# Optimization experiments

Hardware: AMD Instinct MI355X
Metric: run time of the kernel (lower is better)

The kernel has to match this reference:

```python
import jax, jax.numpy as jnp
from jax import lax
import numpy as np

NDIM = 256
BATCH = 65536
NROT = NDIM * (NDIM - 1) // 2  # comb(ndim, 2) = 32640


def _givens_mat(rots, ii, jj, ndim):
    """Product G_last @ ... @ G_1 of Givens rotations in combinations order.

    Left-multiplying by G(i, j, theta) only modifies rows i and j, so we apply
    each rotation as a rank-2 row update instead of a full matmul (same math
    as the original `plane_rot_mat @ mat` loop).
    """
    def step(mat, carry):
        i, j, th = carry
        c = jnp.cos(th)
        s = jnp.sin(th)
        ri = mat[i]
        rj = mat[j]
        mat = mat.at[i].set(c * ri - s * rj)
        mat = mat.at[j].set(s * ri + c * rj)
        return mat, None

    mat0 = jnp.eye(ndim, dtype=jnp.complex64)
    mat, _ = lax.scan(step, mat0, (ii, jj, rots))
    return mat


def setup_inputs() -> dict:
    key = jax.random.key(0)
    k1, k2, k3, k4 = jax.random.split(key, 4)
    x = jax.random.normal(k1, (BATCH, NDIM), dtype=jnp.float32)
    rots1 = 0.1 * jax.random.normal(k2, (NROT,), dtype=jnp.float32)
    phases = 0.1 * jax.random.normal(k3, (NDIM,), dtype=jnp.float32)
    rots2 = 0.1 * jax.random.normal(k4, (NROT,), dtype=jnp.float32)
    return {"x": x, "rots1": rots1, "phases": phases, "rots2": rots2}


def reference(x, rots1, phases, rots2):
    ndim = x.shape[1]
    # np.triu_indices(ndim, 1) enumerates (i, j) pairs in the same row-major
    # order as itertools.combinations(range(ndim), 2).
    ii_np, jj_np = np.triu_indices(ndim, k=1)
    ii = jnp.asarray(ii_np, dtype=jnp.int32)
    jj = jnp.asarray(jj_np, dtype=jnp.int32)

    # vector_norm: row-wise L2 normalization
    xn = x / jnp.linalg.norm(x, axis=1, keepdims=True)
    xc = xn.astype(jnp.complex64)

    # rot1: y = x @ M1.T with M1 = G_last @ ... @ G_1
    M1 = _givens_mat(rots1, ii, jj, ndim)
    y = xc @ M1.T

    # phase_transforms: x @ diag(exp(i*phases)) == elementwise phase multiply
    y = y * jnp.exp(1j * phases)

    # rot2
    M2 = _givens_mat(rots2, ii, jj, ndim)
    y = y @ M2.T

    # measure: |.|^2
    return jnp.abs(y) ** 2
```

## Files before the change

### kernel.cpp

```cpp
#include <hip/hip_runtime.h>
#include <stdint.h>
#include <math.h>

#define NDIM 256
#define BATCH 65536
#define NROT 32640

typedef float  f32x4 __attribute__((ext_vector_type(4)));
typedef short  s16x8 __attribute__((ext_vector_type(8)));
typedef unsigned int u32x4 __attribute__((ext_vector_type(4)));
typedef unsigned int u32x2 __attribute__((ext_vector_type(2)));

static __device__ __forceinline__ unsigned short f2bf(float f) {
    unsigned int u = __float_as_uint(f);
    u += 0x7fffu + ((u >> 16) & 1u);
    return (unsigned short)(u >> 16);
}

static __device__ __forceinline__ int sweep_bound(int k, int pblk) {
    int target = k * (NROT / pblk);
    int best = 0, bd = 0x7fffffff;
    for (int i = 0; i <= 256; i += 4) {
        int pre = i * 255 - (i * (i - 1)) / 2;
        int d = pre - target; d = (d < 0) ? -d : d;
        if (d < bd) { bd = d; best = i; }
    }
    return best;
}

__global__ __launch_bounds__(64) void k_blocks(const float* __restrict__ r1,
                                               const float* __restrict__ r2,
                                               float* __restrict__ bmats, int pblk) {
    __shared__ float colb[264 * 64];
    __shared__ float2 csb[256 * 4];
    __shared__ float2 tri[24 * 6];
    const int t = threadIdx.x;
    const int chunk = blockIdx.x;
    const int b = blockIdx.y;
    const int set = blockIdx.z;
    const int col0 = chunk * 64;
    const float* rots = set ? r2 : r1;

    const int s0 = sweep_bound(b, pblk);
    const int s1 = sweep_bound(b + 1, pblk);
    const int ngroups = (s1 - s0) >> 2;

    {
        const f32x4 z = {0.f, 0.f, 0.f, 0.f};
        #pragma unroll 11
        for (int q = 0; q < 66; q++)
            *(f32x4*)&colb[(q * 64 + t) * 4] = z;
        colb[(col0 + t) * 64 + t] = 1.0f;
    }

    for (int k = t; k < ngroups * 6; k += 64) {
        int g = k / 6, q = k - g * 6;
        int a  = (q < 3) ? 0 : ((q < 5) ? 1 : 2);
        int bb = (q < 3) ? (q + 1) : ((q < 5) ? (q - 1) : 3);
        int m0 = s0 + g * 4;
        int m = m0 + a;
        int base = m * 255 - (m * (m - 1)) / 2;
        float th = rots[base - m - 1 + (m0 + bb)];
        float sv, cv; sincosf(th, &sv, &cv);
        tri[k] = make_float2(cv, sv);
    }

    for (int g = 0; g < ngroups; g++) {
        const int m0 = s0 + g * 4;
        int off[4];
        #pragma unroll
        for (int a = 0; a < 4; a++) {
            int m = m0 + a;
            int base = m * 255 - (m * (m - 1)) / 2;
            off[a] = base - m - 1;
        }
        const int n_j = 252 - m0;
        const int n_p = (n_j > 0) ? ((n_j + 7) & ~7) : 0;

        for (int k = t; k < n_p * 4; k += 64) {
            int jj = k >> 2, a = k & 3;
            int j = m0 + 4 + jj;
            if (j < 256) {
                float th = rots[off[a] + j];
                float sv, cv; sincosf(th, &sv, &cv);
                csb[k] = make_float2(cv, sv);
            } else {
                csb[k] = make_float2(1.f, 0.f);
            }
        }

        float u0 = colb[(m0 + 0) * 64 + t];
        float u1 = colb[(m0 + 1) * 64 + t];
        float u2 = colb[(m0 + 2) * 64 + t];
        float u3 = colb[(m0 + 3) * 64 + t];

        {
            float2 cv; float nr;
            cv = tri[g * 6 + 0]; nr = cv.y * u0 + cv.x * u1; u0 = cv.x * u0 - cv.y * u1; u1 = nr;
            cv = tri[g * 6 + 1]; nr = cv.y * u0 + cv.x * u2; u0 = cv.x * u0 - cv.y * u2; u2 = nr;
            cv = tri[g * 6 + 2]; nr = cv.y * u0 + cv.x * u3; u0 = cv.x * u0 - cv.y * u3; u3 = nr;
            cv = tri[g * 6 + 3]; nr = cv.y * u1 + cv.x * u2; u1 = cv.x * u1 - cv.y * u2; u2 = nr;
            cv = tri[g * 6 + 4]; nr = cv.y * u1 + cv.x * u3; u1 = cv.x * u1 - cv.y * u3; u3 = nr;
            cv = tri[g * 6 + 5]; nr = cv.y * u2 + cv.x * u3; u2 = cv.x * u2 - cv.y * u3; u3 = nr;
        }

        if (n_p > 0) {
            float rbuf[8];
            #pragma unroll
            for (int p = 0; p < 8; p++)
                rbuf[p] = colb[(m0 + 4 + p) * 64 + t];
            for (int c = 0; c < n_p; c += 8) {
                #pragma unroll
                for (int p = 0; p < 8; p++) {
                    const int j = m0 + 4 + c + p;
                    float r = rbuf[p];
                    int jn = j + 8; jn = (jn < 263) ? jn : 263;
                    rbuf[p] = colb[jn * 64 + t];
                    float2 a0 = csb[(c + p) * 4 + 0];
                    float2 a1 = csb[(c + p) * 4 + 1];
                    float2 a2 = csb[(c + p) * 4 + 2];
                    float2 a3 = csb[(c + p) * 4 + 3];
                    float nr;
                    nr = a0.y * u0 + a0.x * r; u0 = a0.x * u0 - a0.y * r; r = nr;
                    nr = a1.y * u1 + a1.x * r; u1 = a1.x * u1 - a1.y * r; r = nr;
                    nr = a2.y * u2 + a2.x * r; u2 = a2.x * u2 - a2.y * r; r = nr;
                    nr = a3.y * u3 + a3.x * r; u3 = a3.x * u3 - a3.y * r; r = nr;
                    colb[j * 64 + t] = r;
                }
            }
        }
        colb[(m0 + 0) * 64 + t] = u0;
        colb[(m0 + 1) * 64 + t] = u1;
        colb[(m0 + 2) * 64 + t] = u2;
        colb[(m0 + 3) * 64 + t] = u3;
    }

    float* outm = bmats + (size_t)(set * pblk + b) * 65536;
    for (int r = 0; r < 256; r++)
        outm[(size_t)r * 256 + col0 + t] = colb[r * 64 + t];
}

__global__ __launch_bounds__(256) void k_combine(const float* __restrict__ src,
                                                 float* __restrict__ dst,
                                                 int half, int pblk) {
    const int by = blockIdx.y;
    const int set = by / half, pidx = by % half;
    const int stride = pblk / (2 * half);
    const int s0A = sweep_bound((2 * pidx + 1) * stride, pblk);
    const float* Am = src + (size_t)(set * 2 * half + 2 * pidx + 1) * 65536;
    const float* Bm = src + (size_t)(set * 2 * half + 2 * pidx) * 65536;
    float* Dm = dst + (size_t)(set * half + pidx) * 65536;
    const int tr = blockIdx.x >> 2, tc = blockIdx.x & 3;
    const int tid = threadIdx.x;

    if (tr * 64 + 64 <= s0A) {
        #pragma unroll
        for (int it = 0; it < 4; it++) {
            int flat = tid + it * 256;
            int r = flat >> 4, c4 = flat & 15;
            size_t idx = (size_t)(tr * 64 + r) * 256 + tc * 64 + c4 * 4;
            *(f32x4*)&Dm[idx] = *(const f32x4*)&Bm[idx];
        }
        return;
    }
    const int kb0 = (tr * 64 >= s0A) ? (s0A >> 5) : 0;

    __shared__ float As[64 * 36];
    __shared__ float Bs[32 * 64];
    const int tx = tid & 15, ty = tid >> 4;

    float acc[4][4] = {};
    for (int kb = kb0; kb < 8; kb++) {
        __syncthreads();
        #pragma unroll
        for (int it = 0; it < 2; it++) {
            int flat = tid + it * 256;
            int r = flat >> 3, c4 = flat & 7;
            f32x4 v = *(const f32x4*)&Am[(size_t)(tr * 64 + r) * 256 + kb * 32 + c4 * 4];
            *(f32x4*)&As[r * 36 + c4 * 4] = v;
        }
        #pragma unroll
        for (int it = 0; it < 2; it++) {
            int flat = tid + it * 256;
            int r = flat >> 4, c4 = flat & 15;
            f32x4 v = *(const f32x4*)&Bm[(size_t)(kb * 32 + r) * 256 + tc * 64 + c4 * 4];
            *(f32x4*)&Bs[r * 64 + c4 * 4] = v;
        }
        __syncthreads();
        #pragma unroll 8
        for (int kk = 0; kk < 32; kk++) {
            f32x4 bv = *(const f32x4*)&Bs[kk * 64 + tx * 4];
            float a0 = As[(ty * 4 + 0) * 36 + kk];
            float a1 = As[(ty * 4 + 1) * 36 + kk];
            float a2 = As[(ty * 4 + 2) * 36 + kk];
            float a3 = As[(ty * 4 + 3) * 36 + kk];
            #pragma unroll
            for (int j = 0; j < 4; j++) {
                acc[0][j] += a0 * bv[j];
                acc[1][j] += a1 * bv[j];
                acc[2][j] += a2 * bv[j];
                acc[3][j] += a3 * bv[j];
            }
        }
    }
    #pragma unroll
    for (int i = 0; i < 4; i++) {
        f32x4 v = { acc[i][0], acc[i][1], acc[i][2], acc[i][3] };
        *(f32x4*)&Dm[(size_t)(tr * 64 + ty * 4 + i) * 256 + tc * 64 + tx * 4] = v;
    }
}

__global__ __launch_bounds__(256) void k_abt(const float* __restrict__ mats,
                                             const float* __restrict__ phases,
                                             unsigned short* __restrict__ abt) {
    const float* Am = mats + 65536;
    const float* Bm = mats;
    const int v = blockIdx.y;
    const int tr = blockIdx.x >> 2, tc = blockIdx.x & 3;

    __shared__ float As[64 * 36];
    __shared__ float Bs[32 * 64];
    const int tid = threadIdx.x;
    const int tx = tid & 15, ty = tid >> 4;

    float acc[4][4] = {};
    for (int kb = 0; kb < 8; kb++) {
        __syncthreads();
        #pragma unroll
        for (int it = 0; it < 2; it++) {
            int flat = tid + it * 256;
            int r = flat >> 3, c4 = flat & 7;
            f32x4 vv = *(const f32x4*)&Am[(size_t)(tr * 64 + r) * 256 + kb * 32 + c4 * 4];
            *(f32x4*)&As[r * 36 + c4 * 4] = vv;
        }
        #pragma unroll
        for (int it = 0; it < 2; it++) {
            int flat = tid + it * 256;
            int r = flat >> 4, c4 = flat & 15;
            int kg = kb * 32 + r;
            float ph = phases[kg];
            float sc = v ? sinf(ph) : cosf(ph);
            f32x4 vv = *(const f32x4*)&Bm[(size_t)kg * 256 + tc * 64 + c4 * 4];
            vv[0] *= sc; vv[1] *= sc; vv[2] *= sc; vv[3] *= sc;
            *(f32x4*)&Bs[r * 64 + c4 * 4] = vv;
        }
        __syncthreads();
        #pragma unroll 8
        for (int kk = 0; kk < 32; kk++) {
            f32x4 bv = *(const f32x4*)&Bs[kk * 64 + tx * 4];
            float a0 = As[(ty * 4 + 0) * 36 + kk];
            float a1 = As[(ty * 4 + 1) * 36 + kk];
            float a2 = As[(ty * 4 + 2) * 36 + kk];
            float a3 = As[(ty * 4 + 3) * 36 + kk];
            #pragma unroll
            for (int j = 0; j < 4; j++) {
                acc[0][j] += a0 * bv[j];
                acc[1][j] += a1 * bv[j];
                acc[2][j] += a2 * bv[j];
                acc[3][j] += a3 * bv[j];
            }
        }
    }
    #pragma unroll
    for (int i = 0; i < 4; i++) {
        unsigned short h0 = f2bf(acc[i][0]), h1 = f2bf(acc[i][1]);
        unsigned short h2 = f2bf(acc[i][2]), h3 = f2bf(acc[i][3]);
        u32x2 pk = { (unsigned)h0 | ((unsigned)h1 << 16),
                     (unsigned)h2 | ((unsigned)h3 << 16) };
        *(u32x2*)&abt[(size_t)(v * 256 + tr * 64 + ty * 4 + i) * 256 + tc * 64 + tx * 4] = pk;
    }
}

__global__ __launch_bounds__(256) void k_xnorm(const float* __restrict__ x,
                                               unsigned short* __restrict__ xbf) {
    const int row = blockIdx.x * 4 + (threadIdx.x >> 6);
    const int lane = threadIdx.x & 63;
    f32x4 v = *(const f32x4*)&x[(size_t)row * 256 + lane * 4];
    float s = v[0] * v[0] + v[1] * v[1] + v[2] * v[2] + v[3] * v[3];
    for (int off = 32; off; off >>= 1) s += __shfl_xor(s, off, 64);
    float sc = 1.0f / sqrtf(s);
    unsigned short h0 = f2bf(v[0] * sc), h1 = f2bf(v[1] * sc);
    unsigned short h2 = f2bf(v[2] * sc), h3 = f2bf(v[3] * sc);
    u32x2 pk = { (unsigned)h0 | ((unsigned)h1 << 16),
                 (unsigned)h2 | ((unsigned)h3 << 16) };
    *(u32x2*)&xbf[(size_t)row * 256 + lane * 4] = pk;
}

__global__ __launch_bounds__(256) void k_norm(const float* __restrict__ x,
                                              float* __restrict__ invn) {
    const int row = blockIdx.x * 4 + (threadIdx.x >> 6);
    const int lane = threadIdx.x & 63;
    f32x4 v = *(const f32x4*)&x[(size_t)row * 256 + lane * 4];
    float s = v[0] * v[0] + v[1] * v[1] + v[2] * v[2] + v[3] * v[3];
    for (int off = 32; off; off >>= 1) s += __shfl_xor(s, off, 64);
    if (lane == 0) invn[row] = 1.0f / sqrtf(s);
}

#define BKP 136
__global__ __launch_bounds__(256) void k_gemm_bf(const unsigned short* __restrict__ xbf,
                                                 const unsigned short* __restrict__ abt,
                                                 float* __restrict__ out) {
    __shared__ unsigned short As[128 * BKP];
    __shared__ unsigned short Bs[128 * BKP];
    const int tid = threadIdx.x;
    const int cb = blockIdx.x;
    const int rb = blockIdx.y;
    const int lane = tid & 63, w = tid >> 6;

    f32x4 acc[16];
    #pragma unroll
    for (int i = 0; i < 16; i++) acc[i] = (f32x4){0.f, 0.f, 0.f, 0.f};

    int rA[8], cA[8], grB[8];
    #pragma unroll
    for (int it = 0; it < 8; it++) {
        int flat = tid + it * 256;
        rA[it] = flat >> 4; cA[it] = flat & 15;
        int r = rA[it];
        grB[it] = (r < 64) ? (cb * 64 + r) : (256 + cb * 64 + (r - 64));
    }

    u32x4 pa[8], pb[8];
    #pragma unroll
    for (int it = 0; it < 8; it++) {
        pa[it] = *(const u32x4*)&xbf[(size_t)(rb * 128 + rA[it]) * 256 + cA[it] * 8];
        pb[it] = *(const u32x4*)&abt[(size_t)grB[it] * 256 + cA[it] * 8];
    }
    #pragma unroll
    for (int it = 0; it < 8; it++) {
        *(u32x4*)&As[rA[it] * BKP + cA[it] * 8] = pa[it];
        *(u32x4*)&Bs[rA[it] * BKP + cA[it] * 8] = pb[it];
    }
    __syncthreads();
    #pragma unroll
    for (int it = 0; it < 8; it++) {
        pa[it] = *(const u32x4*)&xbf[(size_t)(rb * 128 + rA[it]) * 256 + 128 + cA[it] * 8];
        pb[it] = *(const u32x4*)&abt[(size_t)grB[it] * 256 + 128 + cA[it] * 8];
    }

    auto compute = [&]() {
        #pragma unroll
        for (int ks = 0; ks < 4; ks++) {
            const int k0 = ks * 32 + (lane >> 4) * 8;
            s16x8 a[2], b[8];
            #pragma unroll
            for (int tm = 0; tm < 2; tm++)
                a[tm] = *(const s16x8*)&As[(w * 32 + tm * 16 + (lane & 15)) * BKP + k0];
            #pragma unroll
            for (int tn = 0; tn < 8; tn++)
                b[tn] = *(const s16x8*)&Bs[(tn * 16 + (lane & 15)) * BKP + k0];
            #pragma unroll
            for (int tm = 0; tm < 2; tm++)
                #pragma unroll
                for (int tn = 0; tn < 8; tn++)
                    acc[tm * 8 + tn] = __builtin_amdgcn_mfma_f32_16x16x32_bf16(
                        a[tm], b[tn], acc[tm * 8 + tn], 0, 0, 0);
        }
    };
    compute();
    __syncthreads();
    #pragma unroll
    for (int it = 0; it < 8; it++) {
        *(u32x4*)&As[rA[it] * BKP + cA[it] * 8] = pa[it];
        *(u32x4*)&Bs[rA[it] * BKP + cA[it] * 8] = pb[it];
    }
    __syncthreads();
    compute();

    const int qr = lane >> 4, c = lane & 15;
    #pragma unroll
    for (int tm = 0; tm < 2; tm++) {
        #pragma unroll
        for (int tn = 0; tn < 4; tn++) {
            f32x4 p = acc[tm * 8 + tn];
            f32x4 q = acc[tm * 8 + tn + 4];
            #pragma unroll
            for (int r = 0; r < 4; r++) {
                int m = w * 32 + tm * 16 + qr * 4 + r;
                out[(size_t)(rb * 128 + m) * 256 + cb * 64 + tn * 16 + c] =
                    p[r] * p[r] + q[r] * q[r];
            }
        }
    }
}

__global__ __launch_bounds__(256) void k_gemm_f32(const float* __restrict__ x,
                                                  const unsigned short* __restrict__ abt,
                                                  const float* __restrict__ invn,
                                                  float* __restrict__ out) {
    __shared__ unsigned short As[128 * BKP];
    __shared__ unsigned short Bs[128 * BKP];
    const int tid = threadIdx.x;
    const int cb = blockIdx.x;
    const int rb = blockIdx.y;
    const int lane = tid & 63, w = tid >> 6;

    f32x4 acc[16];
    #pragma unroll
    for (int i = 0; i < 16; i++) acc[i] = (f32x4){0.f, 0.f, 0.f, 0.f};

    for (int kb = 0; kb < 2; kb++) {
        __syncthreads();
        #pragma unroll
        for (int it = 0; it < 16; it++) {
            int flat = tid + it * 256;
            int r = flat >> 5, c4 = flat & 31;
            f32x4 v = *(const f32x4*)&x[(size_t)(rb * 128 + r) * 256 + kb * 128 + c4 * 4];
            float sc = invn[rb * 128 + r];
            v[0] *= sc; v[1] *= sc; v[2] *= sc; v[3] *= sc;
            unsigned short h0 = f2bf(v[0]), h1 = f2bf(v[1]);
            unsigned short h2 = f2bf(v[2]), h3 = f2bf(v[3]);
            u32x2 pk = { (unsigned)h0 | ((unsigned)h1 << 16),
                         (unsigned)h2 | ((unsigned)h3 << 16) };
            *(u32x2*)&As[r * BKP + c4 * 4] = pk;
        }
        #pragma unroll
        for (int it = 0; it < 8; it++) {
            int flat = tid + it * 256;
            int r = flat >> 4, c8 = flat & 15;
            int gr = (r < 64) ? (cb * 64 + r) : (256 + cb * 64 + (r - 64));
            u32x4 vv = *(const u32x4*)&abt[(size_t)gr * 256 + kb * 128 + c8 * 8];
            *(u32x4*)&Bs[r * BKP + c8 * 8] = vv;
        }
        __syncthreads();
        #pragma unroll
        for (int ks = 0; ks < 4; ks++) {
            const int k0 = ks * 32 + (lane >> 4) * 8;
            s16x8 a[2], b[8];
            #pragma unroll
            for (int tm = 0; tm < 2; tm++)
                a[tm] = *(const s16x8*)&As[(w * 32 + tm * 16 + (lane & 15)) * BKP + k0];
            #pragma unroll
            for (int tn = 0; tn < 8; tn++)
                b[tn] = *(const s16x8*)&Bs[(tn * 16 + (lane & 15)) * BKP + k0];
            #pragma unroll
            for (int tm = 0; tm < 2; tm++)
                #pragma unroll
                for (int tn = 0; tn < 8; tn++)
                    acc[tm * 8 + tn] = __builtin_amdgcn_mfma_f32_16x16x32_bf16(
                        a[tm], b[tn], acc[tm * 8 + tn], 0, 0, 0);
        }
    }

    const int qr = lane >> 4, c = lane & 15;
    #pragma unroll
    for (int tm = 0; tm < 2; tm++) {
        #pragma unroll
        for (int tn = 0; tn < 4; tn++) {
            f32x4 p = acc[tm * 8 + tn];
            f32x4 q = acc[tm * 8 + tn + 4];
            #pragma unroll
            for (int r = 0; r < 4; r++) {
                int m = w * 32 + tm * 16 + qr * 4 + r;
                out[(size_t)(rb * 128 + m) * 256 + cb * 64 + tn * 16 + c] =
                    p[r] * p[r] + q[r] * q[r];
            }
        }
    }
}

extern "C" void kernel_launch(void* const* d_in, const int* in_sizes, int n_in,
                              void* d_out, int out_size, void* d_ws, size_t ws_size,
                              hipStream_t stream) {
    (void)in_sizes; (void)n_in; (void)out_size;
    const float* x      = (const float*)d_in[0];
    const float* rots1  = (const float*)d_in[1];
    const float* phases = (const float*)d_in[2];
    const float* rots2  = (const float*)d_in[3];
    float* out = (float*)d_out;
    char* ws = (char*)d_ws;

    const size_t MAT = 262144;
    int pblk = 32;
    while (pblk > 16 &&
           (size_t)3 * pblk * MAT + 2 * MAT + (size_t)BATCH * 512 > ws_size)
        pblk >>= 1;
    const size_t offA   = 0;
    const size_t offB   = offA + (size_t)2 * pblk * MAT;
    const size_t offABT = offB + (size_t)pblk * MAT;
    const size_t offINV = offABT + MAT;
    const size_t offXBF = offINV + MAT;
    const bool use_xbf = (offXBF + (size_t)BATCH * 512) <= ws_size;

    float*          A    = (float*)(ws + offA);
    float*          B    = (float*)(ws + offB);
    unsigned short* abt  = (unsigned short*)(ws + offABT);
    float*          invn = (float*)(ws + offINV);
    unsigned short* xbf  = (unsigned short*)(ws + offXBF);

    k_blocks<<<dim3(4, pblk, 2), 64, 0, stream>>>(rots1, rots2, A, pblk);

    float* srcp = A; float* dstp = B;
    for (int half = pblk / 2; half >= 1; half >>= 1) {
        k_combine<<<dim3(16, 2 * half), 256, 0, stream>>>(srcp, dstp, half, pblk);
        float* tmp = srcp; srcp = dstp; dstp = tmp;
    }
    k_abt<<<dim3(16, 2), 256, 0, stream>>>(srcp, phases, abt);

    if (use_xbf) {
        k_xnorm<<<BATCH / 4, 256, 0, stream>>>(x, xbf);
        k_gemm_bf<<<dim3(4, BATCH / 128), 256, 0, stream>>>(xbf, abt, out);
    } else {
        k_norm<<<BATCH / 4, 256, 0, stream>>>(x, invn);
        k_gemm_f32<<<dim3(4, BATCH / 128), 256, 0, stream>>>(x, abt, invn, out);
    }
}
```

Before: 323.1 us.

## Use split-bf16 MFMA in combine/abt GEMMs and fold x normalization into k_blocks

The small 256x256 matrix products in k_combine and k_abt move from scalar FP32 FMA loops to bf16 MFMA instructions. Each operand is split into high and low bf16 parts and three MFMAs are issued per tile, so the products stay close to FP32 accuracy. The row normalization of x is merged into the k_blocks launch as extra blocks, which removes a kernel launch and lets that memory-bound work overlap the serial Givens block computation. This adds split and conversion overhead plus a strided B load, and the three-term split loses some precision compared with FP32.

```diff
diff --git a/kernel.cpp b/kernel.cpp
--- a/kernel.cpp
+++ b/kernel.cpp
@@ -15,6 +15,38 @@
     unsigned int u = __float_as_uint(f);
     u += 0x7fffu + ((u >> 16) & 1u);
     return (unsigned short)(u >> 16);
+}
+static __device__ __forceinline__ float bf2f(unsigned short h) {
+    return __uint_as_float(((unsigned)h) << 16);
+}
+
+static __device__ __forceinline__ void split4(f32x4 v, u32x2* hi, u32x2* lo) {
+    unsigned short h[4], l[4];
+    #pragma unroll
+    for (int i = 0; i < 4; i++) {
+        h[i] = f2bf(v[i]);
+        l[i] = f2bf(v[i] - bf2f(h[i]));
+    }
+    *hi = (u32x2){ (unsigned)h[0] | ((unsigned)h[1] << 16),
+                   (unsigned)h[2] | ((unsigned)h[3] << 16) };
+    *lo = (u32x2){ (unsigned)l[0] | ((unsigned)l[1] << 16),
+                   (unsigned)l[2] | ((unsigned)l[3] << 16) };
+}
+static __device__ __forceinline__ void split8(const float* v, u32x4* hi, u32x4* lo) {
+    unsigned short h[8], l[8];
+    #pragma unroll
+    for (int i = 0; i < 8; i++) {
+        h[i] = f2bf(v[i]);
+        l[i] = f2bf(v[i] - bf2f(h[i]));
+    }
+    *hi = (u32x4){ (unsigned)h[0] | ((unsigned)h[1] << 16),
+                   (unsigned)h[2] | ((unsigned)h[3] << 16),
+                   (unsigned)h[4] | ((unsigned)h[5] << 16),
+                   (unsigned)h[6] | ((unsigned)h[7] << 16) };
+    *lo = (u32x4){ (unsigned)l[0] | ((unsigned)l[1] << 16),
+                   (unsigned)l[2] | ((unsigned)l[3] << 16),
+                   (unsigned)l[4] | ((unsigned)l[5] << 16),
+                   (unsigned)l[6] | ((unsigned)l[7] << 16) };
 }
 
 static __device__ __forceinline__ int sweep_bound(int k, int pblk) {
@@ -30,14 +62,45 @@
 
 __global__ __launch_bounds__(64) void k_blocks(const float* __restrict__ r1,
                                                const float* __restrict__ r2,
-                                               float* __restrict__ bmats, int pblk) {
+                                               float* __restrict__ bmats, int pblk,
+                                               const float* __restrict__ xg,
+                                               unsigned short* __restrict__ xbf) {
     __shared__ float colb[264 * 64];
     __shared__ float2 csb[256 * 4];
     __shared__ float2 tri[24 * 6];
+    const int nblk = 8 * pblk;
+
+    if ((int)blockIdx.x >= nblk) {
+        const int lane = threadIdx.x;
+        const int r0 = ((int)blockIdx.x - nblk) * 16;
+        #pragma unroll
+        for (int hb = 0; hb < 2; hb++) {
+            f32x4 v[8];
+            #pragma unroll
+            for (int i = 0; i < 8; i++)
+                v[i] = *(const f32x4*)&xg[(size_t)(r0 + hb * 8 + i) * 256 + lane * 4];
+            #pragma unroll
+            for (int i = 0; i < 8; i++) {
+                float s = v[i][0] * v[i][0] + v[i][1] * v[i][1]
+                        + v[i][2] * v[i][2] + v[i][3] * v[i][3];
+                #pragma unroll
+                for (int off = 32; off; off >>= 1) s += __shfl_xor(s, off, 64);
+                float sc = 1.0f / sqrtf(s);
+                unsigned short h0 = f2bf(v[i][0] * sc), h1 = f2bf(v[i][1] * sc);
+                unsigned short h2 = f2bf(v[i][2] * sc), h3 = f2bf(v[i][3] * sc);
+                u32x2 pk = { (unsigned)h0 | ((unsigned)h1 << 16),
+                             (unsigned)h2 | ((unsigned)h3 << 16) };
+                *(u32x2*)&xbf[(size_t)(r0 + hb * 8 + i) * 256 + lane * 4] = pk;
+            }
+        }
+        return;
+    }
+
     const int t = threadIdx.x;
-    const int chunk = blockIdx.x;
-    const int b = blockIdx.y;
-    const int set = blockIdx.z;
+    const int bid = blockIdx.x;
+    const int chunk = bid & 3;
+    const int b = (bid >> 2) % pblk;
+    const int set = (bid >> 2) / pblk;
     const int col0 = chunk * 64;
     const float* rots = set ? r2 : r1;
 
@@ -165,11 +228,20 @@
     }
     const int kb0 = (tr * 64 >= s0A) ? (s0A >> 5) : 0;
 
-    __shared__ float As[64 * 36];
-    __shared__ float Bs[32 * 64];
-    const int tx = tid & 15, ty = tid >> 4;
-
-    float acc[4][4] = {};
+    __shared__ unsigned short Ahi[64 * 40], Alo[64 * 40];
+    __shared__ unsigned short Bhi[64 * 40], Blo[64 * 40];
+
+    const int lane = tid & 63, w = tid >> 6;
+    const int mh = (w >> 1) * 32, nh = (w & 1) * 32;
+    const int l15 = lane & 15, lq = lane >> 4;
+    const int bn = tid & 63, bkq = tid >> 6;
+
+    f32x4 acc[2][2];
+    #pragma unroll
+    for (int i = 0; i < 2; i++)
+        #pragma unroll
+        for (int j = 0; j < 2; j++) acc[i][j] = (f32x4){0.f, 0.f, 0.f, 0.f};
+
     for (int kb = kb0; kb < 8; kb++) {
         __syncthreads();
         #pragma unroll
@@ -177,37 +249,48 @@
             int flat = tid + it * 256;
             int r = flat >> 3, c4 = flat & 7;
             f32x4 v = *(const f32x4*)&Am[(size_t)(tr * 64 + r) * 256 + kb * 32 + c4 * 4];
-            *(f32x4*)&As[r * 36 + c4 * 4] = v;
-        }
-        #pragma unroll
-        for (int it = 0; it < 2; it++) {
-            int flat = tid + it * 256;
-            int r = flat >> 4, c4 = flat & 15;
-            f32x4 v = *(const f32x4*)&Bm[(size_t)(kb * 32 + r) * 256 + tc * 64 + c4 * 4];
-            *(f32x4*)&Bs[r * 64 + c4 * 4] = v;
+            u32x2 hi, lo; split4(v, &hi, &lo);
+            *(u32x2*)&Ahi[r * 40 + c4 * 4] = hi;
+            *(u32x2*)&Alo[r * 40 + c4 * 4] = lo;
+        }
+        {
+            float bv[8];
+            #pragma unroll
+            for (int i = 0; i < 8; i++)
+                bv[i] = Bm[(size_t)(kb * 32 + bkq * 8 + i) * 256 + tc * 64 + bn];
+            u32x4 hi, lo; split8(bv, &hi, &lo);
+            *(u32x4*)&Bhi[bn * 40 + bkq * 8] = hi;
+            *(u32x4*)&Blo[bn * 40 + bkq * 8] = lo;
         }
         __syncthreads();
-        #pragma unroll 8
-        for (int kk = 0; kk < 32; kk++) {
-            f32x4 bv = *(const f32x4*)&Bs[kk * 64 + tx * 4];
-            float a0 = As[(ty * 4 + 0) * 36 + kk];
-            float a1 = As[(ty * 4 + 1) * 36 + kk];
-            float a2 = As[(ty * 4 + 2) * 36 + kk];
-            float a3 = As[(ty * 4 + 3) * 36 + kk];
-            #pragma unroll
-            for (int j = 0; j < 4; j++) {
-                acc[0][j] += a0 * bv[j];
-                acc[1][j] += a1 * bv[j];
-                acc[2][j] += a2 * bv[j];
-                acc[3][j] += a3 * bv[j];
-            }
-        }
-    }
-    #pragma unroll
-    for (int i = 0; i < 4; i++) {
-        f32x4 v = { acc[i][0], acc[i][1], acc[i][2], acc[i][3] };
-        *(f32x4*)&Dm[(size_t)(tr * 64 + ty * 4 + i) * 256 + tc * 64 + tx * 4] = v;
-    }
+        s16x8 ah[2], al[2], bh[2], bl[2];
+        #pragma unroll
+        for (int tm = 0; tm < 2; tm++) {
+            ah[tm] = *(const s16x8*)&Ahi[(mh + tm * 16 + l15) * 40 + lq * 8];
+            al[tm] = *(const s16x8*)&Alo[(mh + tm * 16 + l15) * 40 + lq * 8];
+        }
+        #pragma unroll
+        for (int tn = 0; tn < 2; tn++) {
+            bh[tn] = *(const s16x8*)&Bhi[(nh + tn * 16 + l15) * 40 + lq * 8];
+            bl[tn] = *(const s16x8*)&Blo[(nh + tn * 16 + l15) * 40 + lq * 8];
+        }
+        #pragma unroll
+        for (int tm = 0; tm < 2; tm++)
+            #pragma unroll
+            for (int tn = 0; tn < 2; tn++) {
+                acc[tm][tn] = __builtin_amdgcn_mfma_f32_16x16x32_bf16(ah[tm], bh[tn], acc[tm][tn], 0, 0, 0);
+                acc[tm][tn] = __builtin_amdgcn_mfma_f32_16x16x32_bf16(ah[tm], bl[tn], acc[tm][tn], 0, 0, 0);
+                acc[tm][tn] = __builtin_amdgcn_mfma_f32_16x16x32_bf16(al[tm], bh[tn], acc[tm][tn], 0, 0, 0);
+            }
+    }
+    #pragma unroll
+    for (int tm = 0; tm < 2; tm++)
+        #pragma unroll
+        for (int tn = 0; tn < 2; tn++)
+            #pragma unroll
+            for (int r = 0; r < 4; r++)
+                Dm[(size_t)(tr * 64 + mh + tm * 16 + lq * 4 + r) * 256
+                   + tc * 64 + nh + tn * 16 + l15] = acc[tm][tn][r];
 }
 
 __global__ __launch_bounds__(256) void k_abt(const float* __restrict__ mats,
@@ -217,13 +300,22 @@
     const float* Bm = mats;
     const int v = blockIdx.y;
     const int tr = blockIdx.x >> 2, tc = blockIdx.x & 3;
-
-    __shared__ float As[64 * 36];
-    __shared__ float Bs[32 * 64];
     const int tid = threadIdx.x;
-    const int tx = tid & 15, ty = tid >> 4;
-
-    float acc[4][4] = {};
+
+    __shared__ unsigned short Ahi[64 * 40], Alo[64 * 40];
+    __shared__ unsigned short Bhi[64 * 40], Blo[64 * 40];
+
+    const int lane = tid & 63, w = tid >> 6;
+    const int mh = (w >> 1) * 32, nh = (w & 1) * 32;
+    const int l15 = lane & 15, lq = lane >> 4;
+    const int bn = tid & 63, bkq = tid >> 6;
+
+    f32x4 acc[2][2];
+    #pragma unroll
+    for (int i = 0; i < 2; i++)
+        #pragma unroll
+        for (int j = 0; j < 2; j++) acc[i][j] = (f32x4){0.f, 0.f, 0.f, 0.f};
+
     for (int kb = 0; kb < 8; kb++) {
         __syncthreads();
         #pragma unroll
@@ -231,59 +323,52 @@
             int flat = tid + it * 256;
             int r = flat >> 3, c4 = flat & 7;
             f32x4 vv = *(const f32x4*)&Am[(size_t)(tr * 64 + r) * 256 + kb * 32 + c4 * 4];
-            *(f32x4*)&As[r * 36 + c4 * 4] = vv;
-        }
-        #pragma unroll
-        for (int it = 0; it < 2; it++) {
-            int flat = tid + it * 256;
-            int r = flat >> 4, c4 = flat & 15;
-            int kg = kb * 32 + r;
-            float ph = phases[kg];
-            float sc = v ? sinf(ph) : cosf(ph);
-            f32x4 vv = *(const f32x4*)&Bm[(size_t)kg * 256 + tc * 64 + c4 * 4];
-            vv[0] *= sc; vv[1] *= sc; vv[2] *= sc; vv[3] *= sc;
-            *(f32x4*)&Bs[r * 64 + c4 * 4] = vv;
+            u32x2 hi, lo; split4(vv, &hi, &lo);
+            *(u32x2*)&Ahi[r * 40 + c4 * 4] = hi;
+            *(u32x2*)&Alo[r * 40 + c4 * 4] = lo;
+        }
+        {
+            float bv[8];
+            #pragma unroll
+            for (int i = 0; i < 8; i++) {
+                int kg = kb * 32 + bkq * 8 + i;
+                float ph = phases[kg];
+                float sc = v ? sinf(ph) : cosf(ph);
+                bv[i] = Bm[(size_t)kg * 256 + tc * 64 + bn] * sc;
+            }
+            u32x4 hi, lo; split8(bv, &hi, &lo);
+            *(u32x4*)&Bhi[bn * 40 + bkq * 8] = hi;
+            *(u32x4*)&Blo[bn * 40 + bkq * 8] = lo;
         }
         __syncthreads();
-        #pragma unroll 8
-        for (int kk = 0; kk < 32; kk++) {
-            f32x4 bv = *(const f32x4*)&Bs[kk * 64 + tx * 4];
-            float a0 = As[(ty * 4 + 0) * 36 + kk];
-            float a1 = As[(ty * 4 + 1) * 36 + kk];
-            float a2 = As[(ty * 4 + 2) * 36 + kk];
-            float a3 = As[(ty * 4 + 3) * 36 + kk];
-            #pragma unroll
-            for (int j = 0; j < 4; j++) {
-                acc[0][j] += a0 * bv[j];
-                acc[1][j] += a1 * bv[j];
-                acc[2][j] += a2 * bv[j];
-                acc[3][j] += a3 * bv[j];
-            }
-        }
-    }
-    #pragma unroll
-    for (int i = 0; i < 4; i++) {
-        unsigned short h0 = f2bf(acc[i][0]), h1 = f2bf(acc[i][1]);
-        unsigned short h2 = f2bf(acc[i][2]), h3 = f2bf(acc[i][3]);
-        u32x2 pk = { (unsigned)h0 | ((unsigned)h1 << 16),
-                     (unsigned)h2 | ((unsigned)h3 << 16) };
-        *(u32x2*)&abt[(size_t)(v * 256 + tr * 64 + ty * 4 + i) * 256 + tc * 64 + tx * 4] = pk;
-    }
-}
-
-__global__ __launch_bounds__(256) void k_xnorm(const float* __restrict__ x,
-                                               unsigned short* __restrict__ xbf) {
-    const int row = blockIdx.x * 4 + (threadIdx.x >> 6);
-    const int lane = threadIdx.x & 63;
-    f32x4 v = *(const f32x4*)&x[(size_t)row * 256 + lane * 4];
-    float s = v[0] * v[0] + v[1] * v[1] + v[2] * v[2] + v[3] * v[3];
-    for (int off = 32; off; off >>= 1) s += __shfl_xor(s, off, 64);
-    float sc = 1.0f / sqrtf(s);
-    unsigned short h0 = f2bf(v[0] * sc), h1 = f2bf(v[1] * sc);
-    unsigned short h2 = f2bf(v[2] * sc), h3 = f2bf(v[3] * sc);
-    u32x2 pk = { (unsigned)h0 | ((unsigned)h1 << 16),
-                 (unsigned)h2 | ((unsigned)h3 << 16) };
-    *(u32x2*)&xbf[(size_t)row * 256 + lane * 4] = pk;
+        s16x8 ah[2], al[2], bh[2], bl[2];
+        #pragma unroll
+        for (int tm = 0; tm < 2; tm++) {
+            ah[tm] = *(const s16x8*)&Ahi[(mh + tm * 16 + l15) * 40 + lq * 8];
+            al[tm] = *(const s16x8*)&Alo[(mh + tm * 16 + l15) * 40 + lq * 8];
+        }
+        #pragma unroll
+        for (int tn = 0; tn < 2; tn++) {
+            bh[tn] = *(const s16x8*)&Bhi[(nh + tn * 16 + l15) * 40 + lq * 8];
+            bl[tn] = *(const s16x8*)&Blo[(nh + tn * 16 + l15) * 40 + lq * 8];
+        }
+        #pragma unroll
+        for (int tm = 0; tm < 2; tm++)
+            #pragma unroll
+            for (int tn = 0; tn < 2; tn++) {
+                acc[tm][tn] = __builtin_amdgcn_mfma_f32_16x16x32_bf16(ah[tm], bh[tn], acc[tm][tn], 0, 0, 0);
+                acc[tm][tn] = __builtin_amdgcn_mfma_f32_16x16x32_bf16(ah[tm], bl[tn], acc[tm][tn], 0, 0, 0);
+                acc[tm][tn] = __builtin_amdgcn_mfma_f32_16x16x32_bf16(al[tm], bh[tn], acc[tm][tn], 0, 0, 0);
+            }
+    }
+    #pragma unroll
+    for (int tm = 0; tm < 2; tm++)
+        #pragma unroll
+        for (int tn = 0; tn < 2; tn++)
+            #pragma unroll
+            for (int r = 0; r < 4; r++)
+                abt[(size_t)(v * 256 + tr * 64 + mh + tm * 16 + lq * 4 + r) * 256
+                    + tc * 64 + nh + tn * 16 + l15] = f2bf(acc[tm][tn][r]);
 }
 
 __global__ __launch_bounds__(256) void k_norm(const float* __restrict__ x,
@@ -488,7 +573,9 @@
     float*          invn = (float*)(ws + offINV);
     unsigned short* xbf  = (unsigned short*)(ws + offXBF);
 
-    k_blocks<<<dim3(4, pblk, 2), 64, 0, stream>>>(rots1, rots2, A, pblk);
+    const int nblk = 8 * pblk;
+    const int nxn  = use_xbf ? (BATCH / 16) : 0;
+    k_blocks<<<nblk + nxn, 64, 0, stream>>>(rots1, rots2, A, pblk, x, xbf);
 
     float* srcp = A; float* dstp = B;
     for (int half = pblk / 2; half >= 1; half >>= 1) {
@@ -498,7 +585,6 @@
     k_abt<<<dim3(16, 2), 256, 0, stream>>>(srcp, phases, abt);
 
     if (use_xbf) {
-        k_xnorm<<<BATCH / 4, 256, 0, stream>>>(x, xbf);
         k_gemm_bf<<<dim3(4, BATCH / 128), 256, 0, stream>>>(xbf, abt, out);
     } else {
         k_norm<<<BATCH / 4, 256, 0, stream>>>(x, invn);
```

New measurement: 269.7 us. 16.5% less time.
